# Kernel tuning notes

Hardware: AMD Instinct MI355X
Metric: run time of the kernel (lower is better)

## Reference

```python
import jax, jax.numpy as jnp
import numpy as np

B, L, D = 4, 2048, 1024
DI = D            # d_inner = expand * d_model, expand=1
N = 8             # d_state
K = 4             # d_conv
R = 64            # dt_rank = ceil(d_model/16)
EPS = 1e-5


def setup_inputs() -> dict:
    key = jax.random.key(0)
    ks = jax.random.split(key, 10)
    hidden_states = jax.random.normal(ks[0], (B, L, D), dtype=jnp.float32)
    norm_w = jnp.ones((D,), dtype=jnp.float32)
    in_proj_w = jax.random.normal(ks[1], (2 * DI, D), dtype=jnp.float32) * 0.02
    conv_w = jax.random.normal(ks[2], (DI, 1, K), dtype=jnp.float32) * 0.2
    conv_b = jnp.zeros((DI,), dtype=jnp.float32)
    x_proj_w = jax.random.normal(ks[3], (R + 2 * N, DI), dtype=jnp.float32) * 0.02
    dt_proj_w = jax.random.normal(ks[4], (DI, R), dtype=jnp.float32) * 0.1
    # bias init so softplus(bias) lands in a sane dt range (~e^-4 .. e^-1)
    dt_proj_b = jax.random.uniform(ks[5], (DI,), minval=-4.0, maxval=-1.0, dtype=jnp.float32)
    # S4D-real style init: A = -[1..N] per channel
    A_log = jnp.log(jnp.broadcast_to(jnp.arange(1, N + 1, dtype=jnp.float32), (DI, N)))
    D_skip = jnp.ones((DI,), dtype=jnp.float32)
    out_proj_w = jax.random.normal(ks[6], (D, DI), dtype=jnp.float32) * 0.02
    return {
        "hidden_states": hidden_states, "norm_w": norm_w,
        "in_proj_w": in_proj_w, "conv_w": conv_w, "conv_b": conv_b,
        "x_proj_w": x_proj_w, "dt_proj_w": dt_proj_w, "dt_proj_b": dt_proj_b,
        "A_log": A_log, "D_skip": D_skip, "out_proj_w": out_proj_w,
    }


def _rmsnorm(x, w):
    return x * jax.lax.rsqrt(jnp.mean(x * x, axis=-1, keepdims=True) + EPS) * w


def _mamba_block(hidden_states, norm_w, in_proj_w, conv_w, conv_b,
                 x_proj_w, dt_proj_w, dt_proj_b, A_log, D_skip, out_proj_w):
    x = _rmsnorm(hidden_states, norm_w)                      # [B,L,D]
    xz = jnp.einsum('bld,ed->ble', x, in_proj_w)             # [B,L,2*DI]
    x, z = jnp.split(xz, 2, axis=-1)                         # [B,L,DI] each
    # causal depthwise conv1d (torch pads d_conv-1 both sides then slices :L => left pad only)
    xc = jnp.transpose(x, (0, 2, 1))                         # [B,DI,L]
    k = conv_w.shape[-1]
    xc = jax.lax.conv_general_dilated(
        xc, conv_w, window_strides=(1,), padding=[(k - 1, 0)],
        dimension_numbers=('NCH', 'OIH', 'NCH'), feature_group_count=DI)
    x = jax.nn.silu(jnp.transpose(xc, (0, 2, 1)) + conv_b)   # [B,L,DI]
    # input-dependent dt, B, C
    dbl = jnp.einsum('bld,ed->ble', x, x_proj_w)             # [B,L,R+2N]
    dt, Bm, Cm = jnp.split(dbl, [R, R + N], axis=-1)
    dt = jax.nn.softplus(jnp.einsum('blr,dr->bld', dt, dt_proj_w) + dt_proj_b)  # [B,L,DI]
    A = -jnp.exp(A_log)                                      # [DI,N]
    dA = jnp.exp(dt[..., None] * A)                          # [B,L,DI,N]
    dBx = dt[..., None] * Bm[:, :, None, :] * x[..., None]   # [B,L,DI,N]

    def step(h, inp):
        a_t, bx_t, c_t = inp                                 # [B,DI,N],[B,DI,N],[B,N]
        h = a_t * h + bx_t
        y = jnp.einsum('bdn,bn->bd', h, c_t)
        return h, y

    h0 = jnp.zeros((hidden_states.shape[0], DI, N), dtype=x.dtype)
    _, ys = jax.lax.scan(step, h0, (jnp.transpose(dA, (1, 0, 2, 3)),
                                    jnp.transpose(dBx, (1, 0, 2, 3)),
                                    jnp.transpose(Cm, (1, 0, 2))))
    y = jnp.transpose(ys, (1, 0, 2)) + D_skip * x            # [B,L,DI]
    y = y * jax.nn.silu(z)
    out = jnp.einsum('bld,ed->ble', y, out_proj_w)           # [B,L,D]
    return out  # use_res=False


def reference(hidden_states, norm_w, in_proj_w, conv_w, conv_b,
              x_proj_w, dt_proj_w, dt_proj_b, A_log, D_skip, out_proj_w):
    return _mamba_block(hidden_states, norm_w, in_proj_w, conv_w, conv_b,
                        x_proj_w, dt_proj_w, dt_proj_b, A_log, D_skip, out_proj_w)
```

## Files before the change

kernel.cpp:

```cpp
#include <hip/hip_runtime.h>
#include <stdint.h>
#include <stddef.h>


typedef unsigned short u16;
typedef unsigned int u32;
typedef _Float16 f16;
typedef __attribute__((ext_vector_type(8))) _Float16 half8;
typedef __attribute__((ext_vector_type(4))) _Float16 half4;
typedef __attribute__((ext_vector_type(4))) float f32x4;

#define LSEQ 2048
#define DMODEL 1024
#define NSTATE 8
#define NCHUNK 64
#define CHUNKL 32
#define NROWS 8192
#define WS_NEED (115ull << 20)

__device__ __forceinline__ void gload_lds16(const void* g, void* l) {
    __builtin_amdgcn_global_load_lds((__attribute__((address_space(1))) void*)g,
                                     (__attribute__((address_space(3))) void*)l,
                                     16, 0, 0);
}

__global__ __launch_bounds__(256) void sentinel_kernel(float* __restrict__ out, int n) {
    int i = blockIdx.x * 256 + threadIdx.x;
    if (i < n) out[i] = 999.0f;
}

#define T0 524288
#define T1 20480
#define T2 16384
#define T3 262144
#define WCVT_BLK 3216
#define ZERO_BLK 640
__global__ __launch_bounds__(256) void prep_kernel(const float* __restrict__ s0,
                                                   const float* __restrict__ s1,
                                                   const float* __restrict__ s2,
                                                   const float* __restrict__ s3,
                                                   f16* __restrict__ d0, f16* __restrict__ d1,
                                                   f16* __restrict__ d2, f16* __restrict__ d3,
                                                   float* __restrict__ dblz,
                                                   const float* __restrict__ X,
                                                   const float* __restrict__ W,
                                                   f16* __restrict__ O) {
    const int bx = blockIdx.x;
    const int tid = threadIdx.x;
    if (bx < WCVT_BLK) {
        int idx = bx * 256 + tid;
        const float* s; f16* d; int i;
        if (idx < T0) { s = s0; d = d0; i = idx; }
        else if (idx < T0 + T1) { s = s1; d = d1; i = idx - T0; }
        else if (idx < T0 + T1 + T2) { s = s2; d = d2; i = idx - T0 - T1; }
        else { s = s3; d = d3; i = idx - T0 - T1 - T2; }
        f32x4 v = *(const f32x4*)(s + (size_t)i * 4);
        half4 o; o[0] = (f16)v[0]; o[1] = (f16)v[1]; o[2] = (f16)v[2]; o[3] = (f16)v[3];
        *(half4*)(d + (size_t)i * 4) = o;
    } else if (bx < WCVT_BLK + ZERO_BLK) {
        int i = (bx - WCVT_BLK) * 256 + tid;
        const f32x4 z4 = {0.f, 0.f, 0.f, 0.f};
        ((f32x4*)dblz)[i] = z4;
    } else {
        const int row = bx - (WCVT_BLK + ZERO_BLK);
        f32x4 u = *(const f32x4*)(X + (size_t)row * DMODEL + tid * 4);
        float ss = u[0]*u[0] + u[1]*u[1] + u[2]*u[2] + u[3]*u[3];
        for (int off = 32; off; off >>= 1) ss += __shfl_down(ss, off, 64);
        __shared__ float red[4];
        if ((tid & 63) == 0) red[tid >> 6] = ss;
        __syncthreads();
        float tot = red[0] + red[1] + red[2] + red[3];
        float scale = rsqrtf(tot * (1.0f / DMODEL) + 1e-5f);
        f32x4 w = *(const f32x4*)(W + tid * 4);
        half4 o;
        o[0] = (f16)(u[0] * scale * w[0]); o[1] = (f16)(u[1] * scale * w[1]);
        o[2] = (f16)(u[2] * scale * w[2]); o[3] = (f16)(u[3] * scale * w[3]);
        *(half4*)(O + (size_t)row * DMODEL + tid * 4) = o;
    }
}


#define SA8(tt, hf) do { \
    gload_lds16(aG + (size_t)(tt) * 64 + (size_t)(hf) * hA, \
                sA + (((tt) & 1) * 16384) + (hf) * 8192 + ldsW); \
    gload_lds16(aG + (size_t)(tt) * 64 + (size_t)(hf) * hA + rA, \
                sA + (((tt) & 1) * 16384) + (hf) * 8192 + 4096 + ldsW); \
} while (0)
#define SB8(tt, hf) do { \
    gload_lds16(bG + (size_t)(tt) * 64 + (size_t)(hf) * hB, \
                sB + (((tt) & 1) * 16384) + (hf) * 8192 + ldsW); \
    gload_lds16(bG + (size_t)(tt) * 64 + (size_t)(hf) * hB + rB, \
                sB + (((tt) & 1) * 16384) + (hf) * 8192 + 4096 + ldsW); \
} while (0)

template <int EPI>
__global__ __launch_bounds__(512, 2) void gemm1b(const f16* __restrict__ Ap, int lda,
                                                 const f16* __restrict__ Bm, int ldb,
                                                 void* __restrict__ C0, void* __restrict__ C1,
                                                 int KT) {
    __shared__ alignas(16) f16 sA[2 * 256 * 64];
    __shared__ alignas(16) f16 sB[2 * 256 * 64];
    const int tid = threadIdx.x;
    const int wave = tid >> 6, lane = tid & 63;
    const int wm = wave >> 2, wn = wave & 3;
    const int cl = lane & 15, q = lane >> 4;
    const int tm = blockIdx.x, tn = blockIdx.y;

    const int srow = tid >> 3;
    const int skc = (tid & 7) ^ (srow & 7);
    const f16* aG = Ap + (size_t)(tm * 256 + srow) * lda + skc * 8;
    const f16* bG = Bm + (size_t)(tn * 256 + srow) * ldb + skc * 8;
    const size_t rA = (size_t)64 * lda, hA = (size_t)128 * lda;
    const size_t rB = (size_t)64 * ldb, hB = (size_t)128 * ldb;
    const int ldsW = wave * 512;

    const int swz0 = (q ^ (cl & 7)) << 3;
    const int swz1 = ((4 + q) ^ (cl & 7)) << 3;
    const int rdA0 = (wm * 128 + cl) * 64 + swz0;
    const int rdA1 = (wm * 128 + cl) * 64 + swz1;
    const int rdB0 = (wn * 64 + cl) * 64 + swz0;
    const int rdB1 = (wn * 64 + cl) * 64 + swz1;

    f32x4 acc[8][4];
    const f32x4 zero4 = {0.f, 0.f, 0.f, 0.f};
#pragma unroll
    for (int f = 0; f < 8; f++)
#pragma unroll
        for (int g = 0; g < 4; g++) acc[f][g] = zero4;

    SA8(0, 0); SA8(0, 1); SB8(0, 0); SB8(0, 1);
    asm volatile("s_waitcnt vmcnt(0)" ::: "memory");
    __builtin_amdgcn_s_barrier();
    __builtin_amdgcn_sched_barrier(0);

    for (int t = 0; t < KT; t++) {
        const f16* sAb = sA + (t & 1) * 16384;
        const f16* sBb = sB + (t & 1) * 16384;

        if (t + 1 < KT) { SA8(t + 1, 0); SA8(t + 1, 1); SB8(t + 1, 0); SB8(t + 1, 1); }
        __builtin_amdgcn_sched_barrier(0);

        half8 a0[4][2], a1[4][2], b0[2][2], b1[2][2];
#pragma unroll
        for (int f = 0; f < 4; f++) {
            a0[f][0] = *(const half8*)(sAb + rdA0 + f * 1024);
            a0[f][1] = *(const half8*)(sAb + rdA1 + f * 1024);
        }
#pragma unroll
        for (int g = 0; g < 2; g++) {
            b0[g][0] = *(const half8*)(sBb + rdB0 + g * 1024);
            b0[g][1] = *(const half8*)(sBb + rdB1 + g * 1024);
        }
        __builtin_amdgcn_s_setprio(1);
#pragma unroll
        for (int f = 0; f < 4; f++)
#pragma unroll
            for (int g = 0; g < 2; g++) {
                acc[f][g] = __builtin_amdgcn_mfma_f32_16x16x32_f16(a0[f][0], b0[g][0], acc[f][g], 0, 0, 0);
                acc[f][g] = __builtin_amdgcn_mfma_f32_16x16x32_f16(a0[f][1], b0[g][1], acc[f][g], 0, 0, 0);
            }
#pragma unroll
        for (int g = 0; g < 2; g++) {
            b1[g][0] = *(const half8*)(sBb + rdB0 + (2 + g) * 1024);
            b1[g][1] = *(const half8*)(sBb + rdB1 + (2 + g) * 1024);
        }
#pragma unroll
        for (int f = 0; f < 4; f++)
#pragma unroll
            for (int g = 0; g < 2; g++) {
                acc[f][2 + g] = __builtin_amdgcn_mfma_f32_16x16x32_f16(a0[f][0], b1[g][0], acc[f][2 + g], 0, 0, 0);
                acc[f][2 + g] = __builtin_amdgcn_mfma_f32_16x16x32_f16(a0[f][1], b1[g][1], acc[f][2 + g], 0, 0, 0);
            }
#pragma unroll
        for (int f = 0; f < 4; f++) {
            a1[f][0] = *(const half8*)(sAb + rdA0 + (4 + f) * 1024);
            a1[f][1] = *(const half8*)(sAb + rdA1 + (4 + f) * 1024);
        }
#pragma unroll
        for (int f = 0; f < 4; f++)
#pragma unroll
            for (int g = 0; g < 2; g++) {
                acc[4 + f][2 + g] = __builtin_amdgcn_mfma_f32_16x16x32_f16(a1[f][0], b1[g][0], acc[4 + f][2 + g], 0, 0, 0);
                acc[4 + f][2 + g] = __builtin_amdgcn_mfma_f32_16x16x32_f16(a1[f][1], b1[g][1], acc[4 + f][2 + g], 0, 0, 0);
            }
#pragma unroll
        for (int f = 0; f < 4; f++)
#pragma unroll
            for (int g = 0; g < 2; g++) {
                acc[4 + f][g] = __builtin_amdgcn_mfma_f32_16x16x32_f16(a1[f][0], b0[g][0], acc[4 + f][g], 0, 0, 0);
                acc[4 + f][g] = __builtin_amdgcn_mfma_f32_16x16x32_f16(a1[f][1], b0[g][1], acc[4 + f][g], 0, 0, 0);
            }
        __builtin_amdgcn_s_setprio(0);

        if (t + 1 < KT) {
            asm volatile("s_waitcnt vmcnt(0)" ::: "memory");
            __builtin_amdgcn_s_barrier();
            __builtin_amdgcn_sched_barrier(0);
        }
    }

    const int rowb = tm * 256 + wm * 128 + q * 4;
    const int colb = tn * 256 + wn * 64 + cl;
#pragma unroll
    for (int f = 0; f < 8; f++)
#pragma unroll
        for (int r = 0; r < 4; r++) {
            size_t ro = (size_t)(rowb + f * 16 + r) * 1024;
#pragma unroll
            for (int g = 0; g < 4; g++) {
                int gc = colb + g * 16;
                float v = acc[f][g][r];
                if (EPI == 0) {
                    if (gc < 1024) ((f16*)C0)[ro + gc] = (f16)v;
                    else           ((f16*)C1)[ro + gc - 1024] = (f16)v;
                } else {
                    ((float*)C0)[ro + gc] = v;
                }
            }
        }
}

template <int EPI, int AF32>
__global__ __launch_bounds__(256) void gemm_f16(const void* __restrict__ Ap, int lda,
                                                const f16* __restrict__ Bm, int ldb,
                                                void* __restrict__ C0, void* __restrict__ C1,
                                                int ldc, int N, int klen,
                                                const float* __restrict__ fbias) {
    __shared__ alignas(16) f16 sA[128 * 64];
    __shared__ alignas(16) f16 sB[128 * 64];
    const int tid = threadIdx.x;
    const int wave = tid >> 6, lane = tid & 63;
    const int wm = (wave >> 1) * 64, wn = (wave & 1) * 64;
    const int tm = blockIdx.x, tn = blockIdx.y;
    const int q = lane >> 4, cl = lane & 15;
    const int kbeg = blockIdx.z * klen;

    f32x4 acc[4][4];
    const f32x4 zero4 = {0.f, 0.f, 0.f, 0.f};
#pragma unroll
    for (int t = 0; t < 4; t++)
#pragma unroll
        for (int u = 0; u < 4; u++) acc[t][u] = zero4;

    int rS[4], gkS[4];
#pragma unroll
    for (int j = 0; j < 4; j++) {
        int c = wave * 256 + j * 64 + lane;
        rS[j] = c >> 3;
        gkS[j] = (c & 7) ^ (rS[j] & 7);
    }

    for (int k0 = kbeg; k0 < kbeg + klen; k0 += 64) {
        __syncthreads();
#pragma unroll
        for (int j = 0; j < 4; j++) {
            int ldsoff = (wave * 256 + j * 64) * 8;
            if (!AF32) {
                int ga = tm * 128 + rS[j];
                gload_lds16((const f16*)Ap + (size_t)ga * lda + k0 + gkS[j] * 8, sA + ldsoff);
            }
            int gb = tn * 128 + rS[j];
            if (gb >= N) gb = N - 1;
            gload_lds16(Bm + (size_t)gb * ldb + k0 + gkS[j] * 8, sB + ldsoff);
        }
        __syncthreads();

        half8 af[4][2], bf[4][2];
#pragma unroll
        for (int t = 0; t < 4; t++)
#pragma unroll
            for (int s = 0; s < 2; s++) {
                int m = wm + t * 16 + cl;
                int kc = s * 4 + q;
                if (AF32) {
                    const float* pa = (const float*)Ap + (size_t)(tm * 128 + m) * lda + k0 + kc * 8;
                    f32x4 v0 = *(const f32x4*)pa, v1 = *(const f32x4*)(pa + 4);
                    half8 a;
                    a[0] = (f16)v0[0]; a[1] = (f16)v0[1]; a[2] = (f16)v0[2]; a[3] = (f16)v0[3];
                    a[4] = (f16)v1[0]; a[5] = (f16)v1[1]; a[6] = (f16)v1[2]; a[7] = (f16)v1[3];
                    af[t][s] = a;
                } else {
                    af[t][s] = *(const half8*)(sA + m * 64 + ((kc ^ (m & 7)) << 3));
                }
                int n = wn + t * 16 + cl;
                bf[t][s] = *(const half8*)(sB + n * 64 + ((kc ^ (n & 7)) << 3));
            }
#pragma unroll
        for (int t = 0; t < 4; t++)
#pragma unroll
            for (int u = 0; u < 4; u++) {
                acc[t][u] = __builtin_amdgcn_mfma_f32_16x16x32_f16(af[t][0], bf[u][0], acc[t][u], 0, 0, 0);
                acc[t][u] = __builtin_amdgcn_mfma_f32_16x16x32_f16(af[t][1], bf[u][1], acc[t][u], 0, 0, 0);
            }
    }

    const int rowbase = tm * 128 + wm + q * 4;
    const int colbase = tn * 128 + wn + cl;
#pragma unroll
    for (int t = 0; t < 4; t++)
#pragma unroll
        for (int r = 0; r < 4; r++) {
            size_t rb_ = (size_t)(rowbase + t * 16 + r) * ldc;
            size_t rb1 = (size_t)(rowbase + t * 16 + r) * 1024;
#pragma unroll
            for (int u = 0; u < 4; u++) {
                int gcol = colbase + u * 16;
                float v = acc[t][u][r];
                if (EPI == 0) {
                    if (gcol < 1024) ((f16*)C0)[rb1 + gcol] = (f16)v;
                    else             ((f16*)C1)[rb1 + gcol - 1024] = (f16)v;
                } else if (EPI == 1) {
                    if (gcol < N) ((float*)C0)[rb_ + gcol] = v;
                } else if (EPI == 2) {
                    if (gcol < N) atomicAdd((float*)C0 + rb_ + gcol, v);
                } else {
                    if (gcol < N) {
                        float sv = v + fbias[gcol];
                        sv = (sv > 15.f) ? sv : log1pf(__expf(sv));
                        ((f16*)C0)[rb_ + gcol] = (f16)sv;
                    }
                }
            }
        }
}

template __global__ void gemm_f16<3, 1>(const void*, int, const f16*, int,
                                        void*, void*, int, int, int, const float*);
template __global__ void gemm_f16<0, 0>(const void*, int, const f16*, int,
                                        void*, void*, int, int, int, const float*);

__global__ __launch_bounds__(256) void dtproj_kernel(const float* __restrict__ Ap,
                                                     const f16* __restrict__ Wt,
                                                     f16* __restrict__ Cd,
                                                     const float* __restrict__ fbias) {
    __shared__ alignas(16) f16 sW[128 * 64];
    const int tid = threadIdx.x;
    const int wave = tid >> 6, lane = tid & 63;
    const int q = lane >> 4, cl = lane & 15;
    const int tm = blockIdx.x, tn = blockIdx.y;

#pragma unroll
    for (int j = 0; j < 4; j++) {
        int c = wave * 256 + j * 64 + lane;
        int row = c >> 3;
        int kc = (c & 7) ^ (row & 7);
        gload_lds16(Wt + (size_t)(tn * 128 + row) * 64 + kc * 8,
                    sW + (wave * 256 + j * 64) * 8);
    }

    half8 af[2][2];
#pragma unroll
    for (int t = 0; t < 2; t++)
#pragma unroll
        for (int s = 0; s < 2; s++) {
            int m = wave * 32 + t * 16 + cl;
            const float* pa = Ap + (size_t)(tm * 128 + m) * 80 + (s * 4 + q) * 8;
            f32x4 v0 = *(const f32x4*)pa, v1 = *(const f32x4*)(pa + 4);
            half8 a;
            a[0] = (f16)v0[0]; a[1] = (f16)v0[1]; a[2] = (f16)v0[2]; a[3] = (f16)v0[3];
            a[4] = (f16)v1[0]; a[5] = (f16)v1[1]; a[6] = (f16)v1[2]; a[7] = (f16)v1[3];
            af[t][s] = a;
        }

    __syncthreads();

    f32x4 acc[2][8];
    const f32x4 zero4 = {0.f, 0.f, 0.f, 0.f};
#pragma unroll
    for (int t = 0; t < 2; t++)
#pragma unroll
        for (int fn = 0; fn < 8; fn++) acc[t][fn] = zero4;

#pragma unroll
    for (int fn = 0; fn < 8; fn++) {
        int n = fn * 16 + cl;
#pragma unroll
        for (int s = 0; s < 2; s++) {
            half8 bf = *(const half8*)(sW + n * 64 + (((s * 4 + q) ^ (n & 7)) << 3));
            acc[0][fn] = __builtin_amdgcn_mfma_f32_16x16x32_f16(af[0][s], bf, acc[0][fn], 0, 0, 0);
            acc[1][fn] = __builtin_amdgcn_mfma_f32_16x16x32_f16(af[1][s], bf, acc[1][fn], 0, 0, 0);
        }
    }

    const int rowb = tm * 128 + wave * 32 + q * 4;
    const int colb = tn * 128 + cl;
#pragma unroll
    for (int t = 0; t < 2; t++)
#pragma unroll
        for (int r = 0; r < 4; r++) {
            size_t ro = (size_t)(rowb + t * 16 + r) * 1024;
#pragma unroll
            for (int fn = 0; fn < 8; fn++) {
                int gc = colb + fn * 16;
                float sv = acc[t][fn][r] + fbias[gc];
                sv = (sv > 15.f) ? sv : log1pf(__expf(sv));
                Cd[ro + gc] = (f16)sv;
            }
        }
}

__global__ __launch_bounds__(256) void conv_silu_kernel(const f16* __restrict__ x,
                                                        const float* __restrict__ cw,
                                                        const float* __restrict__ cb,
                                                        f16* __restrict__ xc) {
    const int rg = blockIdx.x;
    const int d = blockIdx.y * 256 + threadIdx.x;
    const int row0 = rg * 4;
    const int l0 = row0 & (LSEQ - 1);
    float w0 = cw[d * 4], w1 = cw[d * 4 + 1], w2 = cw[d * 4 + 2], w3 = cw[d * 4 + 3];
    float bias = cb[d];
    float v[7];
#pragma unroll
    for (int j = 0; j < 7; j++) {
        int ll = l0 - 3 + j;
        v[j] = (ll >= 0) ? (float)x[(size_t)(row0 - 3 + j) * 1024 + d] : 0.f;
    }
#pragma unroll
    for (int i = 0; i < 4; i++) {
        float acc = bias + w0 * v[i] + w1 * v[i + 1] + w2 * v[i + 2] + w3 * v[i + 3];
        xc[(size_t)(row0 + i) * 1024 + d] = (f16)(acc / (1.f + __expf(-acc)));
    }
}

__global__ __launch_bounds__(256) void scan1_kernel(const f16* __restrict__ dt,
                                                    const f16* __restrict__ xc,
                                                    const float* __restrict__ dbl,
                                                    const float* __restrict__ A_log,
                                                    float* __restrict__ hF,
                                                    float* __restrict__ Pb) {
    const int d = blockIdx.x * 256 + threadIdx.x;
    const int c = blockIdx.y;
    const int b = blockIdx.z;
    __shared__ float sB[CHUNKL * NSTATE];
    sB[threadIdx.x] = dbl[(size_t)(b * LSEQ + c * CHUNKL + (threadIdx.x >> 3)) * 80 + 64 + (threadIdx.x & 7)];
    __syncthreads();
    f32x4 al0 = *(const f32x4*)(A_log + d * 8);
    f32x4 al1 = *(const f32x4*)(A_log + d * 8 + 4);
    float Aa[NSTATE];
#pragma unroll
    for (int n = 0; n < 4; n++) { Aa[n] = -__expf(al0[n]); Aa[n + 4] = -__expf(al1[n]); }
    float h[NSTATE], P[NSTATE];
#pragma unroll
    for (int n = 0; n < NSTATE; n++) { h[n] = 0.f; P[n] = 1.f; }
    const f16* pdt = dt + (size_t)(b * LSEQ + c * CHUNKL) * 1024 + d;
    const f16* pxc = xc + (size_t)(b * LSEQ + c * CHUNKL) * 1024 + d;
    for (int lb = 0; lb < CHUNKL; lb += 8) {
        float vdt[8], vxc[8];
#pragma unroll
        for (int j = 0; j < 8; j++) {
            vdt[j] = (float)pdt[(size_t)(lb + j) * 1024];
            vxc[j] = (float)pxc[(size_t)(lb + j) * 1024];
        }
#pragma unroll
        for (int j = 0; j < 8; j++) {
            float dtx = vdt[j] * vxc[j];
#pragma unroll
            for (int n = 0; n < NSTATE; n++) {
                float e = __expf(Aa[n] * vdt[j]);
                h[n] = e * h[n] + dtx * sB[(lb + j) * 8 + n];
                P[n] *= e;
            }
        }
    }
    size_t base = ((size_t)(c * 4 + b) * 1024 + d) * 8;
    f32x4 o;
    o[0]=h[0]; o[1]=h[1]; o[2]=h[2]; o[3]=h[3]; *(f32x4*)(hF + base) = o;
    o[0]=h[4]; o[1]=h[5]; o[2]=h[6]; o[3]=h[7]; *(f32x4*)(hF + base + 4) = o;
    o[0]=P[0]; o[1]=P[1]; o[2]=P[2]; o[3]=P[3]; *(f32x4*)(Pb + base) = o;
    o[0]=P[4]; o[1]=P[5]; o[2]=P[6]; o[3]=P[7]; *(f32x4*)(Pb + base + 4) = o;
}

__global__ __launch_bounds__(256) void combine_kernel(const float* __restrict__ hF,
                                                      const float* __restrict__ Pb,
                                                      float* __restrict__ h0) {
    int t = blockIdx.x * 256 + threadIdx.x;
    int n = t & 7, dd = (t >> 3) & 1023, b = t >> 13;
    size_t off = (size_t)(b * 1024 + dd) * 8 + n;
    float h = 0.f;
#pragma unroll 8
    for (int c = 0; c < NCHUNK; c++) {
        size_t idx = (size_t)c * 32768 + off;
        h0[idx] = h;
        h = fmaf(Pb[idx], h, hF[idx]);
    }
}

__global__ __launch_bounds__(256) void scan2_kernel(const f16* __restrict__ dt,
                                                    const f16* __restrict__ xc,
                                                    const float* __restrict__ dbl,
                                                    const float* __restrict__ A_log,
                                                    const float* __restrict__ h0,
                                                    const f16* __restrict__ z,
                                                    const float* __restrict__ Dsk,
                                                    f16* __restrict__ yout) {
    const int d = blockIdx.x * 256 + threadIdx.x;
    const int c = blockIdx.y;
    const int b = blockIdx.z;
    __shared__ float sB[CHUNKL * NSTATE];
    __shared__ float sC[CHUNKL * NSTATE];
    {
        size_t rb = (size_t)(b * LSEQ + c * CHUNKL + (threadIdx.x >> 3)) * 80;
        sB[threadIdx.x] = dbl[rb + 64 + (threadIdx.x & 7)];
        sC[threadIdx.x] = dbl[rb + 72 + (threadIdx.x & 7)];
    }
    __syncthreads();
    f32x4 al0 = *(const f32x4*)(A_log + d * 8);
    f32x4 al1 = *(const f32x4*)(A_log + d * 8 + 4);
    float Aa[NSTATE];
#pragma unroll
    for (int n = 0; n < 4; n++) { Aa[n] = -__expf(al0[n]); Aa[n + 4] = -__expf(al1[n]); }
    float h[NSTATE];
    {
        size_t base = ((size_t)(c * 4 + b) * 1024 + d) * 8;
        f32x4 h0a = *(const f32x4*)(h0 + base);
        f32x4 h0b = *(const f32x4*)(h0 + base + 4);
#pragma unroll
        for (int n = 0; n < 4; n++) { h[n] = h0a[n]; h[n + 4] = h0b[n]; }
    }
    const float dval = Dsk[d];
    const size_t rowoff = (size_t)(b * LSEQ + c * CHUNKL) * 1024 + d;
    const f16* pdt = dt + rowoff;
    const f16* pxc = xc + rowoff;
    const f16* pz  = z  + rowoff;
    f16* py = yout + rowoff;
    for (int lb = 0; lb < CHUNKL; lb += 8) {
        float vdt[8], vxc[8], vz[8];
#pragma unroll
        for (int j = 0; j < 8; j++) {
            vdt[j] = (float)pdt[(size_t)(lb + j) * 1024];
            vxc[j] = (float)pxc[(size_t)(lb + j) * 1024];
            vz[j]  = (float)pz[(size_t)(lb + j) * 1024];
        }
#pragma unroll
        for (int j = 0; j < 8; j++) {
            float dtx = vdt[j] * vxc[j];
            float y = 0.f;
#pragma unroll
            for (int n = 0; n < NSTATE; n++) {
                float e = __expf(Aa[n] * vdt[j]);
                h[n] = e * h[n] + dtx * sB[(lb + j) * 8 + n];
                y += h[n] * sC[(lb + j) * 8 + n];
            }
            y += dval * vxc[j];
            y *= vz[j] / (1.f + __expf(-vz[j]));
            py[(size_t)(lb + j) * 1024] = (f16)y;
        }
    }
}

extern "C" void kernel_launch(void* const* d_in, const int* in_sizes, int n_in,
                              void* d_out, int out_size, void* d_ws, size_t ws_size,
                              hipStream_t stream) {
    (void)in_sizes; (void)n_in;
    const float* hidden    = (const float*)d_in[0];
    const float* norm_w    = (const float*)d_in[1];
    const float* in_proj_w = (const float*)d_in[2];
    const float* conv_w    = (const float*)d_in[3];
    const float* conv_b    = (const float*)d_in[4];
    const float* x_proj_w  = (const float*)d_in[5];
    const float* dt_proj_w = (const float*)d_in[6];
    const float* dt_proj_b = (const float*)d_in[7];
    const float* A_log     = (const float*)d_in[8];
    const float* D_skip    = (const float*)d_in[9];
    const float* out_proj_w= (const float*)d_in[10];
    float* out = (float*)d_out;

    if (ws_size < WS_NEED) {
        sentinel_kernel<<<dim3((out_size + 255) / 256), 256, 0, stream>>>(out, out_size);
        return;
    }

    char* ws = (char*)d_ws;
    f16*   xn_h  = (f16*)(ws);
    f16*   xbuf_h= (f16*)(ws + (16ull << 20));
    f16*   zbuf_h= (f16*)(ws + (32ull << 20));
    f16*   xc_h  = (f16*)(ws + (48ull << 20));
    f16*   wih   = (f16*)(ws + (64ull << 20));
    f16*   woh   = (f16*)(ws + (68ull << 20));
    f16*   wxh   = (f16*)(ws + (70ull << 20));
    f16*   wdh   = (f16*)(ws + (70ull << 20) + (512ull << 10));
    float* dbl_f = (float*)(ws + (71ull << 20));
    f16*   dth   = (f16*)(ws + (75ull << 20));
    float* hF    = (float*)(ws + (91ull << 20));
    float* Pb    = (float*)(ws + (99ull << 20));
    float* h0    = (float*)(ws + (107ull << 20));
    f16*   y_h   = xn_h;

    prep_kernel<<<dim3(WCVT_BLK + ZERO_BLK + NROWS), 256, 0, stream>>>(
        in_proj_w, x_proj_w, dt_proj_w, out_proj_w, wih, wxh, wdh, woh,
        dbl_f, hidden, norm_w, xn_h);
    gemm1b<0><<<dim3(32, 8), 512, 0, stream>>>(xn_h, 1024, wih, 1024,
                                               xbuf_h, zbuf_h, 16);
    conv_silu_kernel<<<dim3(NROWS / 4, 4), 256, 0, stream>>>(xbuf_h, conv_w, conv_b, xc_h);
    gemm_f16<2, 0><<<dim3(64, 1, 4), 256, 0, stream>>>(xc_h, 1024, wxh, 1024,
                                                       dbl_f, nullptr, 80, 80, 256, nullptr);
    dtproj_kernel<<<dim3(64, 8), 256, 0, stream>>>(dbl_f, wdh, dth, dt_proj_b);
    scan1_kernel<<<dim3(4, NCHUNK, 4), 256, 0, stream>>>(dth, xc_h, dbl_f, A_log, hF, Pb);
    combine_kernel<<<dim3(128), 256, 0, stream>>>(hF, Pb, h0);
    scan2_kernel<<<dim3(4, NCHUNK, 4), 256, 0, stream>>>(dth, xc_h, dbl_f, A_log, h0,
                                                         zbuf_h, D_skip, y_h);
    gemm_f16<1, 0><<<dim3(64, 8), 256, 0, stream>>>(y_h, 1024, woh, 1024,
                                                    out, nullptr, 1024, 1024, 1024, nullptr);
}
```

Before: 283.7 us.

## Fuse dt projection GEMM and softplus into first chunked scan kernel

Result: slower. 306.4 us (+8.0%).

```diff
diff --git a/kernel.cpp b/kernel.cpp
--- a/kernel.cpp
+++ b/kernel.cpp
@@ -422,18 +422,84 @@
     }
 }
 
-__global__ __launch_bounds__(256) void scan1_kernel(const f16* __restrict__ dt,
-                                                    const f16* __restrict__ xc,
-                                                    const float* __restrict__ dbl,
-                                                    const float* __restrict__ A_log,
-                                                    float* __restrict__ hF,
-                                                    float* __restrict__ Pb) {
-    const int d = blockIdx.x * 256 + threadIdx.x;
+__global__ __launch_bounds__(256) void scan1f_kernel(const f16* __restrict__ xc,
+                                                     const float* __restrict__ dbl,
+                                                     const f16* __restrict__ Wt,
+                                                     const float* __restrict__ fbias,
+                                                     const float* __restrict__ A_log,
+                                                     float* __restrict__ hF,
+                                                     float* __restrict__ Pb,
+                                                     f16* __restrict__ dth) {
+    const int dblk = blockIdx.x;
     const int c = blockIdx.y;
     const int b = blockIdx.z;
+    const int tid = threadIdx.x;
+    const int wave = tid >> 6, lane = tid & 63;
+    const int q = lane >> 4, cl = lane & 15;
+
+    __shared__ alignas(16) f16 sW[256 * 64];
+    __shared__ f16 sDT[32 * 264];
     __shared__ float sB[CHUNKL * NSTATE];
-    sB[threadIdx.x] = dbl[(size_t)(b * LSEQ + c * CHUNKL + (threadIdx.x >> 3)) * 80 + 64 + (threadIdx.x & 7)];
+
+#pragma unroll
+    for (int j = 0; j < 8; j++) {
+        int cidx = j * 256 + tid;
+        int row = cidx >> 3;
+        int kc = (cidx & 7) ^ (row & 7);
+        gload_lds16(Wt + (size_t)(dblk * 256 + row) * 64 + kc * 8, sW + cidx * 8);
+    }
+    sB[tid] = dbl[(size_t)(b * LSEQ + c * CHUNKL + (tid >> 3)) * 80 + 64 + (tid & 7)];
+
+    const size_t grow0 = (size_t)b * LSEQ + (size_t)c * CHUNKL;
+    half8 af[2][2];
+#pragma unroll
+    for (int t = 0; t < 2; t++)
+#pragma unroll
+        for (int s = 0; s < 2; s++) {
+            const float* pa = dbl + (grow0 + t * 16 + cl) * 80 + (s * 4 + q) * 8;
+            f32x4 v0 = *(const f32x4*)pa, v1 = *(const f32x4*)(pa + 4);
+            half8 a;
+            a[0] = (f16)v0[0]; a[1] = (f16)v0[1]; a[2] = (f16)v0[2]; a[3] = (f16)v0[3];
+            a[4] = (f16)v1[0]; a[5] = (f16)v1[1]; a[6] = (f16)v1[2]; a[7] = (f16)v1[3];
+            af[t][s] = a;
+        }
+
     __syncthreads();
+
+    f32x4 acc[2][4];
+    const f32x4 zero4 = {0.f, 0.f, 0.f, 0.f};
+#pragma unroll
+    for (int t = 0; t < 2; t++)
+#pragma unroll
+        for (int fn = 0; fn < 4; fn++) acc[t][fn] = zero4;
+#pragma unroll
+    for (int fn = 0; fn < 4; fn++) {
+        int n = wave * 64 + fn * 16 + cl;
+#pragma unroll
+        for (int s = 0; s < 2; s++) {
+            half8 bf = *(const half8*)(sW + n * 64 + (((s * 4 + q) ^ (n & 7)) << 3));
+            acc[0][fn] = __builtin_amdgcn_mfma_f32_16x16x32_f16(af[0][s], bf, acc[0][fn], 0, 0, 0);
+            acc[1][fn] = __builtin_amdgcn_mfma_f32_16x16x32_f16(af[1][s], bf, acc[1][fn], 0, 0, 0);
+        }
+    }
+#pragma unroll
+    for (int t = 0; t < 2; t++)
+#pragma unroll
+        for (int r = 0; r < 4; r++) {
+            int lrow = t * 16 + q * 4 + r;
+#pragma unroll
+            for (int fn = 0; fn < 4; fn++) {
+                int dl = wave * 64 + fn * 16 + cl;
+                float sv = acc[t][fn][r] + fbias[dblk * 256 + dl];
+                sv = (sv > 15.f) ? sv : log1pf(__expf(sv));
+                f16 hv = (f16)sv;
+                sDT[lrow * 264 + dl] = hv;
+                dth[(grow0 + lrow) * 1024 + dblk * 256 + dl] = hv;
+            }
+        }
+    __syncthreads();
+
+    const int d = dblk * 256 + tid;
     f32x4 al0 = *(const f32x4*)(A_log + d * 8);
     f32x4 al1 = *(const f32x4*)(A_log + d * 8 + 4);
     float Aa[NSTATE];
@@ -442,13 +508,12 @@
     float h[NSTATE], P[NSTATE];
 #pragma unroll
     for (int n = 0; n < NSTATE; n++) { h[n] = 0.f; P[n] = 1.f; }
-    const f16* pdt = dt + (size_t)(b * LSEQ + c * CHUNKL) * 1024 + d;
-    const f16* pxc = xc + (size_t)(b * LSEQ + c * CHUNKL) * 1024 + d;
+    const f16* pxc = xc + grow0 * 1024 + d;
     for (int lb = 0; lb < CHUNKL; lb += 8) {
         float vdt[8], vxc[8];
 #pragma unroll
         for (int j = 0; j < 8; j++) {
-            vdt[j] = (float)pdt[(size_t)(lb + j) * 1024];
+            vdt[j] = (float)sDT[(lb + j) * 264 + tid];
             vxc[j] = (float)pxc[(size_t)(lb + j) * 1024];
         }
 #pragma unroll
@@ -594,8 +659,8 @@
     conv_silu_kernel<<<dim3(NROWS / 4, 4), 256, 0, stream>>>(xbuf_h, conv_w, conv_b, xc_h);
     gemm_f16<2, 0><<<dim3(64, 1, 4), 256, 0, stream>>>(xc_h, 1024, wxh, 1024,
                                                        dbl_f, nullptr, 80, 80, 256, nullptr);
-    dtproj_kernel<<<dim3(64, 8), 256, 0, stream>>>(dbl_f, wdh, dth, dt_proj_b);
-    scan1_kernel<<<dim3(4, NCHUNK, 4), 256, 0, stream>>>(dth, xc_h, dbl_f, A_log, hF, Pb);
+    scan1f_kernel<<<dim3(4, NCHUNK, 4), 256, 0, stream>>>(xc_h, dbl_f, wdh, dt_proj_b,
+                                                          A_log, hF, Pb, dth);
     combine_kernel<<<dim3(128), 256, 0, stream>>>(hF, Pb, h0);
     scan2_kernel<<<dim3(4, NCHUNK, 4), 256, 0, stream>>>(dth, xc_h, dbl_f, A_log, h0,
                                                          zbuf_h, D_skip, y_h);
```
